# Performance work log

Hardware: AMD Instinct MI355X
Metric: run time of the kernel (lower is better)

## Reference

```python
import jax, jax.numpy as jnp
import numpy as np

TOP_K = 2
NUM_EXPERTS = 8
CAPACITY_FACTOR = 1.0


def setup_inputs() -> dict:
    key = jax.random.key(0)
    k1, k2, k3, k4 = jax.random.split(key, 4)
    sl, bs, hs, ffn = 2048, 2, 1024, 4096
    x = jax.random.normal(k1, (sl, bs, hs), dtype=jnp.float32)
    router_w = jax.random.normal(k2, (hs, NUM_EXPERTS), dtype=jnp.float32) * 0.02
    w1 = jax.random.normal(k3, (NUM_EXPERTS, hs, ffn), dtype=jnp.float32) * 0.02
    w2 = jax.random.normal(k4, (NUM_EXPERTS, ffn, hs), dtype=jnp.float32) * 0.02
    bias = jnp.zeros((1, 1, hs), dtype=jnp.float32)
    return {"x": x, "router_w": router_w, "w1": w1, "w2": w2, "bias": bias}


def _moe_forward(x, router_w, w1, w2):
    sl, bs, hs = x.shape
    xf = x.reshape(-1, hs)                                   # [T, H]
    T = xf.shape[0]
    TK = T * TOP_K
    capacity = int(CAPACITY_FACTOR * TOP_K * T / NUM_EXPERTS)  # static

    # Router: softmax over experts, then top-k (LearnedRouter)
    scores = jax.nn.softmax(xf @ router_w, axis=-1)          # [T, E]
    expert_weights, top_experts = jax.lax.top_k(scores, TOP_K)  # [T, K]
    ew = expert_weights.reshape(-1)                          # [T*K]
    te = top_experts.reshape(-1).astype(jnp.int32)           # [T*K]

    # indices_and_bins: stable sort by expert id + histogram + inclusive cumsum
    indices = jnp.argsort(te, stable=True)                   # sorted pos -> flat slot
    tokens_per_expert = jnp.zeros((NUM_EXPERTS,), jnp.int32).at[te].add(1)
    bins = jnp.cumsum(tokens_per_expert)                     # inclusive cumsum
    starts = bins - tokens_per_expert                        # exclusive offsets

    # binned_gather -> [E, capacity, H]; tokens beyond capacity are dropped
    c_range = jnp.arange(capacity)
    pos = starts[:, None] + c_range[None, :]                 # [E, C] positions in sorted order
    valid = c_range[None, :] < tokens_per_expert[:, None]    # [E, C]
    slot = indices[jnp.clip(pos, 0, TK - 1)]                 # flat (token*K + k) slot
    tok = slot // TOP_K                                      # source token row
    gathered = jnp.where(valid[..., None], xf[tok], 0.0)     # [E, C, H]

    # grouped expert MLP: gelu(x @ w1) @ w2  (megablocks mlp.MLP)
    h = jax.nn.gelu(jnp.einsum('ech,ehf->ecf', gathered, w1))
    y = jnp.einsum('ecf,efh->ech', h, w2)                    # [E, C, H]

    # binned_scatter: weighted accumulate back to token rows
    p = jnp.arange(TK)
    e_of_p = jnp.searchsorted(bins, p, side='right')         # expert of sorted pos
    c_of_p = p - starts[e_of_p]                              # slot within expert bin
    ok = c_of_p < capacity                                   # dropped tokens contribute 0
    vals = jnp.where(ok[:, None], y[e_of_p, jnp.clip(c_of_p, 0, capacity - 1)], 0.0)
    flat = indices                                           # flat slot at sorted pos p
    w = ew[flat]
    out = jnp.zeros((T, hs), x.dtype).at[flat // TOP_K].add(w[:, None] * vals)
    return out.reshape(sl, bs, hs)


def reference(x, router_w, w1, w2, bias):
    out = _moe_forward(x, router_w, w1, w2)
    return (out, bias)
```

## Files before the change

kernel.cpp:

```cpp
#include <hip/hip_runtime.h>
#include <hip/hip_bf16.h>


#define T_TOK 4096
#define HS 1024
#define FFN 4096
#define NE 8
#define CAP 1024
#define TKS 8192

#define WS_TE   67108864
#define WS_EW   67141632
#define WS_PERM 67174400
#define WS_WT   67239936
#define WS_XB   134348800

typedef float f4 __attribute__((ext_vector_type(4)));
typedef __bf16 bf16x8 __attribute__((ext_vector_type(8)));
typedef float f32x4 __attribute__((ext_vector_type(4)));

__device__ __forceinline__ void gld_lds16(const void* g, void* l) {
    __builtin_amdgcn_global_load_lds(
        (const __attribute__((address_space(1))) unsigned int*)g,
        (__attribute__((address_space(3))) unsigned int*)l, 16, 0, 0);
}

__device__ __forceinline__ bf16x8 ds_read16(const void* p) {
    bf16x8 r;
    unsigned off = (unsigned)(size_t)(const __attribute__((address_space(3))) char*)p;
    asm volatile("ds_read_b128 %0, %1" : "=&v"(r) : "v"(off));
    return r;
}

__global__ void init_out_kernel(float* __restrict__ out, const float* __restrict__ bias) {
    int i = blockIdx.x * 256 + threadIdx.x;
    const int TH = T_TOK * HS;
    if (i < TH) out[i] = 0.0f;
    else if (i < TH + HS) out[i] = bias[i - TH];
}

__global__ __launch_bounds__(256) void router_kernel(const float* __restrict__ x,
                                                     const float* __restrict__ rw,
                                                     int* __restrict__ te,
                                                     float* __restrict__ ew,
                                                     __bf16* __restrict__ xb) {
    __shared__ float rwt[NE * HS];
    int tid = threadIdx.x;
    for (int i = tid; i < NE * HS; i += 256) {
        int h = i >> 3, e = i & 7;
        rwt[e * HS + h] = rw[i];
    }
    __syncthreads();
    int wave = tid >> 6, lane = tid & 63;
    int t = blockIdx.x * 4 + wave;
    const float* xr = x + (size_t)t * HS;
    float s[NE];
    float xv[16];
#pragma unroll
    for (int e = 0; e < NE; ++e) s[e] = 0.0f;
#pragma unroll
    for (int j = 0; j < 16; ++j) {
        int h = lane + j * 64;
        xv[j] = xr[h];
#pragma unroll
        for (int e = 0; e < NE; ++e) s[e] += xv[j] * rwt[e * HS + h];
    }
#pragma unroll
    for (int j = 0; j < 16; ++j)
        xb[(size_t)t * HS + lane + j * 64] = (__bf16)xv[j];
#pragma unroll
    for (int e = 0; e < NE; ++e) {
#pragma unroll
        for (int off = 1; off < 64; off <<= 1) s[e] += __shfl_xor(s[e], off, 64);
    }
    float m = s[0];
#pragma unroll
    for (int e = 1; e < NE; ++e) m = fmaxf(m, s[e]);
    float psum = 0.0f;
#pragma unroll
    for (int e = 0; e < NE; ++e) psum += __expf(s[e] - m);
    int e0 = 0; float v0 = s[0];
#pragma unroll
    for (int e = 1; e < NE; ++e) { if (s[e] > v0) { v0 = s[e]; e0 = e; } }
    int e1 = -1; float v1 = -1e30f;
#pragma unroll
    for (int e = 0; e < NE; ++e) { if (e != e0 && s[e] > v1) { v1 = s[e]; e1 = e; } }
    if (lane == 0) {
        float inv = 1.0f / psum;
        te[2 * t]     = e0;
        te[2 * t + 1] = e1;
        ew[2 * t]     = __expf(v0 - m) * inv;
        ew[2 * t + 1] = __expf(v1 - m) * inv;
    }
}

__global__ __launch_bounds__(256) void sort_kernel(const int* __restrict__ te,
                                                   int* __restrict__ perm) {
    __shared__ int hist[256 * NE];
    int tid = threadIdx.x;
#pragma unroll
    for (int e = 0; e < NE; ++e) hist[tid * NE + e] = 0;
    for (int i = tid; i < TKS; i += 256) perm[i] = -1;
    __syncthreads();
    for (int j = 0; j < 32; ++j) {
        int p = tid * 32 + j;
        hist[tid * NE + te[p]]++;
    }
    __syncthreads();
    if (tid < NE) {
        int run = 0;
        for (int i = 0; i < 256; ++i) {
            int v = hist[i * NE + tid];
            hist[i * NE + tid] = run;
            run += v;
        }
    }
    __syncthreads();
    for (int j = 0; j < 32; ++j) {
        int p = tid * 32 + j;
        int e = te[p];
        int c = hist[tid * NE + e]++;
        if (c < CAP) perm[e * CAP + c] = p;
    }
}

__global__ __launch_bounds__(256) void conv_wt_kernel(const float* __restrict__ w,
                                                      __bf16* __restrict__ wt,
                                                      int K, int N) {
    __shared__ __bf16 t[64][72];
    const int e = blockIdx.z;
    const int kb = blockIdx.y * 64, nb = blockIdx.x * 64;
    const int tid = threadIdx.x;
    const float* src = w + ((size_t)e * K + kb) * N + nb;
    {
        const int kk = tid >> 4, nc = (tid & 15) * 4;
#pragma unroll
        for (int i = 0; i < 4; ++i) {
            int k = kk + 16 * i;
            f4 v = *(const f4*)(src + (size_t)k * N + nc);
            t[nc + 0][k] = (__bf16)v[0];
            t[nc + 1][k] = (__bf16)v[1];
            t[nc + 2][k] = (__bf16)v[2];
            t[nc + 3][k] = (__bf16)v[3];
        }
    }
    __syncthreads();
    __bf16* dst = wt + ((size_t)e * N + nb) * K + kb;
    const int nn = tid >> 3, ch = (tid & 7) * 8;
#pragma unroll
    for (int i = 0; i < 2; ++i) {
        int n = nn + 32 * i;
        bf16x8 v = *(const bf16x8*)(&t[n][ch]);
        *(bf16x8*)(dst + (size_t)n * K + ch) = v;
    }
}


#define PBAR() do {                                                         \
    asm volatile("" ::: "memory");                                          \
    __builtin_amdgcn_s_barrier();                                           \
    asm volatile("" ::: "memory");                                          \
} while (0)

#define WAITV(N_) asm volatile("s_waitcnt vmcnt(" #N_ ")" ::: "memory")

#define LGKM0() do {                                                        \
    asm volatile("s_waitcnt lgkmcnt(0)" ::: "memory");                      \
    __builtin_amdgcn_sched_barrier(0);                                      \
} while (0)

#define STAGE_A(cb_, h_, koff_) do {                                        \
    gld_lds16(aptr[(h_)*2 + 0] + (koff_), &As[cb_][(h_)*128 + w*16 + 0][0]);\
    gld_lds16(aptr[(h_)*2 + 1] + (koff_), &As[cb_][(h_)*128 + w*16 + 8][0]);\
} while (0)

#define STAGE_B(cb_, h_, koff_) do {                                        \
    gld_lds16(bptr[(h_)*2 + 0] + (koff_), &Bs[cb_][(h_)*128 + w*16 + 0][0]);\
    gld_lds16(bptr[(h_)*2 + 1] + (koff_), &Bs[cb_][(h_)*128 + w*16 + 8][0]);\
} while (0)

#define RD_A4(MB_) do {                                                     \
    _Pragma("unroll")                                                       \
    for (int mi = 0; mi < 4; ++mi)                                          \
        _Pragma("unroll")                                                   \
        for (int kk = 0; kk < 2; ++kk)                                      \
            a[mi][kk] = ds_read16(&As[c][wr*128 + ((MB_)+mi)*16 + l15]      \
                            [(((kk*4 + (lane>>4)) ^ (lane&7)) * 8)]);       \
} while (0)

#define RD_B2(NB_) do {                                                     \
    _Pragma("unroll")                                                       \
    for (int ni = 0; ni < 2; ++ni)                                          \
        _Pragma("unroll")                                                   \
        for (int kk = 0; kk < 2; ++kk)                                      \
            b[(NB_)+ni][kk] = ds_read16(&Bs[c][wc*64 + ((NB_)+ni)*16 + l15] \
                            [(((kk*4 + (lane>>4)) ^ (lane&7)) * 8)]);       \
} while (0)

#define MFMA16(MB_, NB_) do {                                               \
    __builtin_amdgcn_s_setprio(1);                                          \
    _Pragma("unroll")                                                       \
    for (int mi = 0; mi < 4; ++mi)                                          \
        _Pragma("unroll")                                                   \
        for (int ni = 0; ni < 2; ++ni)                                      \
            _Pragma("unroll")                                               \
            for (int kk = 0; kk < 2; ++kk)                                  \
                acc[(MB_)+mi][(NB_)+ni] = __builtin_amdgcn_mfma_f32_16x16x32_bf16(\
                    a[mi][kk], b[(NB_)+ni][kk], acc[(MB_)+mi][(NB_)+ni], 0, 0, 0);\
    __builtin_amdgcn_s_setprio(0);                                          \
} while (0)

#define KLOOP(NT_)                                                          \
    STAGE_B(0, 0, 0); STAGE_B(0, 1, 0);                                     \
    STAGE_A(0, 0, 0); STAGE_A(0, 1, 0);                                     \
    STAGE_B(1, 0, 64); STAGE_B(1, 1, 64);                                   \
    STAGE_A(1, 0, 64);                                                      \
    for (int t = 0; t < (NT_); ++t) {                                       \
        const int c = t & 1, o = c ^ 1;                                     \
        if (t == (NT_) - 1) WAITV(0); else WAITV(6);                        \
        PBAR();                                                             \
                   \
        RD_A4(0); RD_B2(0);                                                 \
        if (t + 1 < (NT_)) STAGE_A(o, 1, (t + 1) * 64);                     \
        PBAR(); LGKM0();                                                    \
        MFMA16(0, 0);                                                       \
        PBAR();                                                             \
                                                  \
        RD_B2(2);                                                           \
        PBAR(); LGKM0();                                                    \
        MFMA16(0, 2);                                                       \
        PBAR();                                                             \
               \
        RD_A4(4);                                                           \
        if (t + 2 < (NT_)) STAGE_B(c, 0, (t + 2) * 64);                     \
        PBAR(); LGKM0();                                                    \
        MFMA16(4, 2);                                                       \
        PBAR();                                                             \
                     \
        if (t + 2 < (NT_)) { STAGE_B(c, 1, (t + 2) * 64);                   \
                             STAGE_A(c, 0, (t + 2) * 64); }                 \
        PBAR();                                                             \
        MFMA16(4, 0);                                                       \
        PBAR();                                                             \
    }

__global__ __launch_bounds__(512, 2) void gemm1_kernel(const __bf16* __restrict__ xb,
                                                       const __bf16* __restrict__ w1t,
                                                       const int* __restrict__ perm,
                                                       __bf16* __restrict__ hbuf) {
    __shared__ __bf16 As[2][256][64];
    __shared__ __bf16 Bs[2][256][64];
    const int hw = blockIdx.x + 16 * blockIdx.y + 64 * blockIdx.z;
    const int logical = (hw & 7) * 64 + (hw >> 3);
    const int nblk = logical & 15;
    const int mblk = (logical >> 4) & 3;
    const int e    = logical >> 6;
    const int tid = threadIdx.x, lane = tid & 63, w = tid >> 6;
    const int wr = w >> 2, wc = w & 3;
    const int l15 = lane & 15;
    const int srl = lane >> 3;
    const int gsrc = (lane & 7) ^ srl;

    const __bf16* aptr[4];
    const __bf16* bptr[4];
#pragma unroll
    for (int h = 0; h < 2; ++h) {
#pragma unroll
        for (int o2 = 0; o2 < 2; ++o2) {
            int r = h * 128 + w * 16 + o2 * 8 + srl;
            int p = perm[e * CAP + mblk * 256 + r];
            int tok = (p < 0) ? 0 : (p >> 1);
            aptr[h * 2 + o2] = xb + (size_t)tok * HS + gsrc * 8;
            int brow = nblk * 256 + r;
            bptr[h * 2 + o2] = w1t + ((size_t)e * FFN + brow) * HS + gsrc * 8;
        }
    }

    f32x4 acc[8][4];
#pragma unroll
    for (int mi = 0; mi < 8; ++mi)
#pragma unroll
        for (int ni = 0; ni < 4; ++ni) acc[mi][ni] = (f32x4)0.0f;
    bf16x8 a[4][2], b[4][2];

    KLOOP(HS / 64)

    const int mbase = mblk * 256 + wr * 128;
    const int nbase = nblk * 256 + wc * 64;
#pragma unroll
    for (int mi = 0; mi < 8; ++mi) {
#pragma unroll
        for (int ni = 0; ni < 4; ++ni) {
#pragma unroll
            for (int reg = 0; reg < 4; ++reg) {
                int mrow = mbase + mi * 16 + (lane >> 4) * 4 + reg;
                int ncol = nbase + ni * 16 + l15;
                float z = acc[mi][ni][reg];
                float z2 = z * z;
                float y = z * (1.5957691216057308f + 0.07135481627f * z2);
                float ex = __expf(-y);
                float gv = z * __builtin_amdgcn_rcpf(1.0f + ex);
                hbuf[(size_t)(e * CAP + mrow) * FFN + ncol] = (__bf16)gv;
            }
        }
    }
}

__global__ __launch_bounds__(512, 2) void gemm2_kernel(const __bf16* __restrict__ hbuf,
                                                       const __bf16* __restrict__ w2t,
                                                       const int* __restrict__ perm,
                                                       const float* __restrict__ ew,
                                                       float* __restrict__ out) {
    __shared__ __bf16 As[2][256][64];
    __shared__ __bf16 Bs[2][256][64];
    const int hw = blockIdx.x + 4 * blockIdx.y + 16 * blockIdx.z;
    const int logical = (hw & 7) * 32 + (hw >> 3);
    const int nblk = logical & 3;
    const int mblk = (logical >> 2) & 3;
    const int zz   = logical >> 4;
    const int e    = zz >> 1, half = zz & 1;
    const int tid = threadIdx.x, lane = tid & 63, w = tid >> 6;
    const int wr = w >> 2, wc = w & 3;
    const int l15 = lane & 15;
    const int srl = lane >> 3;
    const int gsrc = (lane & 7) ^ srl;
    const size_t kbase = (size_t)half * 2048;

    const __bf16* aptr[4];
    const __bf16* bptr[4];
#pragma unroll
    for (int h = 0; h < 2; ++h) {
#pragma unroll
        for (int o2 = 0; o2 < 2; ++o2) {
            int r = h * 128 + w * 16 + o2 * 8 + srl;
            aptr[h * 2 + o2] = hbuf + ((size_t)(e * CAP + mblk * 256 + r)) * FFN
                               + kbase + gsrc * 8;
            int brow = nblk * 256 + r;
            bptr[h * 2 + o2] = w2t + ((size_t)e * HS + brow) * FFN
                               + kbase + gsrc * 8;
        }
    }

    f32x4 acc[8][4];
#pragma unroll
    for (int mi = 0; mi < 8; ++mi)
#pragma unroll
        for (int ni = 0; ni < 4; ++ni) acc[mi][ni] = (f32x4)0.0f;
    bf16x8 a[4][2], b[4][2];

    KLOOP(2048 / 64)

    __syncthreads();
    int* sperm = (int*)&As[0][0][0];
    float* swt = (float*)(sperm + 256);
    if (tid < 256) {
        int p = perm[e * CAP + mblk * 256 + tid];
        sperm[tid] = p;
        swt[tid] = (p >= 0) ? ew[p] : 0.0f;
    }
    __syncthreads();

    const int nbase = nblk * 256 + wc * 64;
#pragma unroll
    for (int mi = 0; mi < 8; ++mi) {
#pragma unroll
        for (int reg = 0; reg < 4; ++reg) {
            int mloc = wr * 128 + mi * 16 + (lane >> 4) * 4 + reg;
            int p = sperm[mloc];
            if (p >= 0) {
                int tok = p >> 1;
                float wgt = swt[mloc];
#pragma unroll
                for (int ni = 0; ni < 4; ++ni) {
                    int n = nbase + ni * 16 + l15;
                    atomicAdd(&out[(size_t)tok * HS + n], wgt * acc[mi][ni][reg]);
                }
            }
        }
    }
}

extern "C" void kernel_launch(void* const* d_in, const int* in_sizes, int n_in,
                              void* d_out, int out_size, void* d_ws, size_t ws_size,
                              hipStream_t stream) {
    const float* x    = (const float*)d_in[0];
    const float* rw   = (const float*)d_in[1];
    const float* w1   = (const float*)d_in[2];
    const float* w2   = (const float*)d_in[3];
    const float* bias = (const float*)d_in[4];
    float* out = (float*)d_out;
    char* ws = (char*)d_ws;

    __bf16* hbuf = (__bf16*)ws;
    int*    te   = (int*)(ws + WS_TE);
    float*  ew   = (float*)(ws + WS_EW);
    int*    perm = (int*)(ws + WS_PERM);
    __bf16* wt   = (__bf16*)(ws + WS_WT);
    __bf16* xb   = (__bf16*)(ws + WS_XB);

    hipLaunchKernelGGL(init_out_kernel, dim3((T_TOK * HS + HS + 255) / 256), dim3(256),
                       0, stream, out, bias);
    hipLaunchKernelGGL(router_kernel, dim3(T_TOK / 4), dim3(256), 0, stream,
                       x, rw, te, ew, xb);
    hipLaunchKernelGGL(sort_kernel, dim3(1), dim3(256), 0, stream, te, perm);
    hipLaunchKernelGGL(conv_wt_kernel, dim3(FFN / 64, HS / 64, NE), dim3(256),
                       0, stream, w1, wt, HS, FFN);
    hipLaunchKernelGGL(gemm1_kernel, dim3(FFN / 256, CAP / 256, NE), dim3(512),
                       0, stream, xb, wt, perm, hbuf);
    hipLaunchKernelGGL(conv_wt_kernel, dim3(HS / 64, FFN / 64, NE), dim3(256),
                       0, stream, w2, wt, FFN, HS);
    hipLaunchKernelGGL(gemm2_kernel, dim3(HS / 256, CAP / 256, NE * 2), dim3(512),
                       0, stream, hbuf, wt, perm, ew, out);
}
```

Measured before the change: 276.6 us.

## Fuse w2 transpose-convert into gemm1 epilogue to drop separate conversion launch

Moves the fp32-to-bf16 transpose of w2 into the tail of gemm1: after writing its GELU output, each of the 512 blocks converts 16 64x64 tiles of w2 through LDS into a separate workspace region. The separate w2 conversion kernel is skipped when the workspace is large enough, removing one launch and the serialization between it and gemm1. The cost is that gemm1's blocks carry extra memory-bound work at their end, and the path depends on the workspace size being sufficient, otherwise it falls back to the old kernel.

```diff
diff --git a/kernel.cpp b/kernel.cpp
--- a/kernel.cpp
+++ b/kernel.cpp
@@ -14,6 +14,8 @@
 #define WS_PERM 67174400
 #define WS_WT   67239936
 #define WS_XB   134348800
+#define WS_W2T  142737408
+#define WS_W2T_END (WS_W2T + 67108864)
 
 typedef float f4 __attribute__((ext_vector_type(4)));
 typedef __bf16 bf16x8 __attribute__((ext_vector_type(8)));
@@ -219,24 +221,20 @@
         const int c = t & 1, o = c ^ 1;                                     \
         if (t == (NT_) - 1) WAITV(0); else WAITV(6);                        \
         PBAR();                                                             \
-                   \
         RD_A4(0); RD_B2(0);                                                 \
         if (t + 1 < (NT_)) STAGE_A(o, 1, (t + 1) * 64);                     \
         PBAR(); LGKM0();                                                    \
         MFMA16(0, 0);                                                       \
         PBAR();                                                             \
-                                                  \
         RD_B2(2);                                                           \
         PBAR(); LGKM0();                                                    \
         MFMA16(0, 2);                                                       \
         PBAR();                                                             \
-               \
         RD_A4(4);                                                           \
         if (t + 2 < (NT_)) STAGE_B(c, 0, (t + 2) * 64);                     \
         PBAR(); LGKM0();                                                    \
         MFMA16(4, 2);                                                       \
         PBAR();                                                             \
-                     \
         if (t + 2 < (NT_)) { STAGE_B(c, 1, (t + 2) * 64);                   \
                              STAGE_A(c, 0, (t + 2) * 64); }                 \
         PBAR();                                                             \
@@ -247,11 +245,14 @@
 __global__ __launch_bounds__(512, 2) void gemm1_kernel(const __bf16* __restrict__ xb,
                                                        const __bf16* __restrict__ w1t,
                                                        const int* __restrict__ perm,
-                                                       __bf16* __restrict__ hbuf) {
+                                                       __bf16* __restrict__ hbuf,
+                                                       const float* __restrict__ w2,
+                                                       __bf16* __restrict__ w2t,
+                                                       int fused) {
     __shared__ __bf16 As[2][256][64];
     __shared__ __bf16 Bs[2][256][64];
-    const int hw = blockIdx.x + 16 * blockIdx.y + 64 * blockIdx.z;
-    const int logical = (hw & 7) * 64 + (hw >> 3);
+    const int bid = blockIdx.x + 16 * blockIdx.y + 64 * blockIdx.z;
+    const int logical = (bid & 7) * 64 + (bid >> 3);
     const int nblk = logical & 15;
     const int mblk = (logical >> 4) & 3;
     const int e    = logical >> 6;
@@ -302,6 +303,39 @@
                 float gv = z * __builtin_amdgcn_rcpf(1.0f + ex);
                 hbuf[(size_t)(e * CAP + mrow) * FFN + ncol] = (__bf16)gv;
             }
+        }
+    }
+
+    if (fused) {
+        __syncthreads();
+        __bf16 (*ct)[72] = (__bf16(*)[72])(&As[0][0][0]);
+        for (int q = 0; q < 16; ++q) {
+            int ctile = bid * 16 + q;
+            int ce = ctile >> 10, r = ctile & 1023;
+            int kb = r >> 4, nb = r & 15;
+            const float* src = w2 + (size_t)ce * FFN * HS
+                               + (size_t)(kb * 64) * HS + nb * 64;
+            {
+                const int kk = tid >> 4, nc = (tid & 15) * 4;
+#pragma unroll
+                for (int i = 0; i < 2; ++i) {
+                    int k = kk + 32 * i;
+                    f4 v = *(const f4*)(src + (size_t)k * HS + nc);
+                    ct[nc + 0][k] = (__bf16)v[0];
+                    ct[nc + 1][k] = (__bf16)v[1];
+                    ct[nc + 2][k] = (__bf16)v[2];
+                    ct[nc + 3][k] = (__bf16)v[3];
+                }
+            }
+            __syncthreads();
+            __bf16* dst = w2t + (size_t)ce * HS * FFN
+                          + (size_t)(nb * 64) * FFN + kb * 64;
+            const int nn = tid >> 3, ch = (tid & 7) * 8;
+            {
+                bf16x8 v = *(const bf16x8*)(&ct[nn][ch]);
+                *(bf16x8*)(dst + (size_t)nn * FFN + ch) = v;
+            }
+            __syncthreads();
         }
     }
 }
@@ -397,6 +431,10 @@
     int*    perm = (int*)(ws + WS_PERM);
     __bf16* wt   = (__bf16*)(ws + WS_WT);
     __bf16* xb   = (__bf16*)(ws + WS_XB);
+    __bf16* w2t  = (__bf16*)(ws + WS_W2T);
+
+    const int fused = (ws_size >= (size_t)WS_W2T_END) ? 1 : 0;
+    __bf16* w2dst = fused ? w2t : wt;
 
     hipLaunchKernelGGL(init_out_kernel, dim3((T_TOK * HS + HS + 255) / 256), dim3(256),
                        0, stream, out, bias);
@@ -406,9 +444,10 @@
     hipLaunchKernelGGL(conv_wt_kernel, dim3(FFN / 64, HS / 64, NE), dim3(256),
                        0, stream, w1, wt, HS, FFN);
     hipLaunchKernelGGL(gemm1_kernel, dim3(FFN / 256, CAP / 256, NE), dim3(512),
-                       0, stream, xb, wt, perm, hbuf);
-    hipLaunchKernelGGL(conv_wt_kernel, dim3(HS / 64, FFN / 64, NE), dim3(256),
-                       0, stream, w2, wt, FFN, HS);
+                       0, stream, xb, wt, perm, hbuf, w2, w2t, fused);
+    if (!fused)
+        hipLaunchKernelGGL(conv_wt_kernel, dim3(HS / 64, FFN / 64, NE), dim3(256),
+                           0, stream, w2, wt, FFN, HS);
     hipLaunchKernelGGL(gemm2_kernel, dim3(HS / 256, CAP / 256, NE * 2), dim3(512),
-                       0, stream, hbuf, wt, perm, ew, out);
-}
+                       0, stream, hbuf, w2dst, perm, ew, out);
+}
```

Measured after the change: 287.0 us. 3.8% more time.
